# Kernel optimization log

Hardware: AMD Instinct MI355X
Metric: run time of the kernel (lower is better)

Reference implementation:

```python
import jax, jax.numpy as jnp
import numpy as np

M, A, E, H = 2048, 64, 128, 256
NUM_BOND_TYPES, NUM_ATOM_TYPES = 4, 118

def setup_inputs() -> dict:
    key = jax.random.key(0)
    ks = jax.random.split(key, 12)
    s = 0.02
    return {
        'node_rep': jax.random.normal(ks[0], (M, A, H), jnp.float32),
        'edge_index': jax.random.randint(ks[1], (M, 2, E), 0, A, jnp.int32),
        'bond_type_target': jax.random.randint(ks[2], (M, E), 0, NUM_BOND_TYPES, jnp.int32),
        'atom_type_target': jax.random.randint(ks[3], (M, A), 0, NUM_ATOM_TYPES, jnp.int32),
        'Wp1': jax.random.normal(ks[4], (H, H), jnp.float32) * s, 'bp1': jnp.zeros((H,), jnp.float32),
        'Wp2': jax.random.normal(ks[5], (H, H), jnp.float32) * s, 'bp2': jnp.zeros((H,), jnp.float32),
        'Wb1': jax.random.normal(ks[6], (2 * H, H), jnp.float32) * s, 'bb1': jnp.zeros((H,), jnp.float32),
        'Wb2': jax.random.normal(ks[7], (H, NUM_BOND_TYPES), jnp.float32) * s, 'bb2': jnp.zeros((NUM_BOND_TYPES,), jnp.float32),
        'Wa1': jax.random.normal(ks[8], (H, H), jnp.float32) * s, 'ba1': jnp.zeros((H,), jnp.float32),
        'Wa2': jax.random.normal(ks[9], (H, NUM_ATOM_TYPES), jnp.float32) * s, 'ba2': jnp.zeros((NUM_ATOM_TYPES,), jnp.float32),
    }

def _mlp(x, W1, b1, W2, b2):
    return jnp.maximum(x @ W1 + b1, 0.0) @ W2 + b2

def reference(node_rep, edge_index, bond_type_target, atom_type_target,
              Wp1, bp1, Wp2, bp2, Wb1, bb1, Wb2, bb2, Wa1, ba1, Wa2, ba2):
    # bond_if_proj: per-atom 2-layer MLP (dropout=0 -> identity)  [M,A,H]
    proj = _mlp(node_rep, Wp1, bp1, Wp2, bp2)
    # gather bond endpoint reps: index_select over atoms per molecule  [M,E,H]
    start = jnp.take_along_axis(proj, edge_index[:, 0, :, None], axis=1)
    end = jnp.take_along_axis(proj, edge_index[:, 1, :, None], axis=1)
    bt_in = jnp.concatenate([start, end], axis=-1)            # [M,E,2H]
    bt_logits = _mlp(bt_in, Wb1, bb1, Wb2, bb2)               # [M,E,4]
    bt_logp = jax.nn.log_softmax(bt_logits, axis=-1)
    # per-molecule mean CE averaged over molecules == global mean (equal sizes)
    bond_type_loss = -jnp.mean(jnp.take_along_axis(bt_logp, bond_type_target[..., None], axis=-1))
    bond_type_acc = jnp.mean((jnp.argmax(bt_logits, axis=-1) == bond_type_target).astype(jnp.float32))
    # atom type classifier on raw node reps  [M,A,118]
    at_logits = _mlp(node_rep, Wa1, ba1, Wa2, ba2)
    at_logp = jax.nn.log_softmax(at_logits, axis=-1)
    atom_type_loss = -jnp.mean(jnp.take_along_axis(at_logp, atom_type_target[..., None], axis=-1))
    atom_type_acc = jnp.mean((jnp.argmax(at_logits, axis=-1) == atom_type_target).astype(jnp.float32))
    loss = 0.5 * bond_type_loss + 0.5 * atom_type_loss
    return loss, bond_type_acc, atom_type_acc
```

## Files before the change

kernel.cpp:

```cpp
#include <hip/hip_runtime.h>
#include <hip/hip_bf16.h>

typedef __bf16 bf16x8 __attribute__((ext_vector_type(8)));
typedef float f32x16 __attribute__((ext_vector_type(16)));

__device__ inline unsigned short f2bf(float f) {
  __hip_bfloat16 h = __float2bfloat16(f);
  return *reinterpret_cast<unsigned short*>(&h);
}
__device__ inline unsigned pack2bf(float a, float b) {
  return (unsigned)f2bf(a) | ((unsigned)f2bf(b) << 16);
}
__device__ inline uint2 pack4bf(float a, float b, float c, float d) {
  uint2 r; r.x = pack2bf(a, b); r.y = pack2bf(c, d); return r;
}
__device__ inline bf16x8 as_bf16x8(uint4 v) { return __builtin_bit_cast(bf16x8, v); }
__device__ inline float bitf(unsigned u) { return __builtin_bit_cast(float, u); }
__device__ inline f32x16 mfma16(bf16x8 a, bf16x8 b, f32x16 c) {
  return __builtin_amdgcn_mfma_f32_32x32x16_bf16(a, b, c, 0, 0, 0);
}

#define BADDR(XB, R, KK)                                                       \
  ((XB) + (((((R) * 32 + l31) << 9) + ((KK) << 5) + (h << 4)) ^ swz))

#define GEMMM(XB, W1PTR, W2PTR, CW_)                                           \
  {                                                                            \
    const unsigned char* w1_ = (const unsigned char*)(W1PTR) +                 \
                               (((CW_) + l31) << 5) + (h << 4);                \
    const unsigned char* w2_ = (const unsigned char*)(W2PTR) +                 \
                               (((CW_) + l31) << 5) + (h << 4);                \
    u00 = zero; u01 = zero; u10 = zero; u11 = zero;                            \
    v00 = zero; v01 = zero; v10 = zero; v11 = zero;                            \
    bf16x8 pB0 = *(const bf16x8*)BADDR(XB, 0, 0);                              \
    bf16x8 pB1 = *(const bf16x8*)BADDR(XB, 1, 0);                              \
    uint4 pA0 = *(const uint4*)(w1_ + 0);                                      \
    uint4 pA1 = *(const uint4*)(w1_ + 1024);                                   \
    uint4 pC0 = *(const uint4*)(w2_ + 0);                                      \
    uint4 pC1 = *(const uint4*)(w2_ + 1024);                                   \
    _Pragma("clang loop unroll(disable)")                                      \
    for (int kk = 0; kk < 16; kk += 2) {                                       \
      bf16x8 qB0 = *(const bf16x8*)BADDR(XB, 0, kk + 1);                       \
      bf16x8 qB1 = *(const bf16x8*)BADDR(XB, 1, kk + 1);                       \
      uint4 qA0 = *(const uint4*)(w1_ + ((kk + 1) << 13));                     \
      uint4 qA1 = *(const uint4*)(w1_ + ((kk + 1) << 13) + 1024);              \
      uint4 qC0 = *(const uint4*)(w2_ + ((kk + 1) << 13));                     \
      uint4 qC1 = *(const uint4*)(w2_ + ((kk + 1) << 13) + 1024);              \
      u00 = mfma16(as_bf16x8(pA0), pB0, u00);                                  \
      u10 = mfma16(as_bf16x8(pA1), pB0, u10);                                  \
      u01 = mfma16(as_bf16x8(pA0), pB1, u01);                                  \
      u11 = mfma16(as_bf16x8(pA1), pB1, u11);                                  \
      v00 = mfma16(as_bf16x8(pC0), pB0, v00);                                  \
      v10 = mfma16(as_bf16x8(pC1), pB0, v10);                                  \
      v01 = mfma16(as_bf16x8(pC0), pB1, v01);                                  \
      v11 = mfma16(as_bf16x8(pC1), pB1, v11);                                  \
      if (kk + 2 < 16) {                                                       \
        pB0 = *(const bf16x8*)BADDR(XB, 0, kk + 2);                            \
        pB1 = *(const bf16x8*)BADDR(XB, 1, kk + 2);                            \
        pA0 = *(const uint4*)(w1_ + ((kk + 2) << 13));                         \
        pA1 = *(const uint4*)(w1_ + ((kk + 2) << 13) + 1024);                  \
        pC0 = *(const uint4*)(w2_ + ((kk + 2) << 13));                         \
        pC1 = *(const uint4*)(w2_ + ((kk + 2) << 13) + 1024);                  \
      }                                                                        \
      u00 = mfma16(as_bf16x8(qA0), qB0, u00);                                  \
      u10 = mfma16(as_bf16x8(qA1), qB0, u10);                                  \
      u01 = mfma16(as_bf16x8(qA0), qB1, u01);                                  \
      u11 = mfma16(as_bf16x8(qA1), qB1, u11);                                  \
      v00 = mfma16(as_bf16x8(qC0), qB0, v00);                                  \
      v10 = mfma16(as_bf16x8(qC1), qB0, v10);                                  \
      v01 = mfma16(as_bf16x8(qC0), qB1, v01);                                  \
      v11 = mfma16(as_bf16x8(qC1), qB1, v11);                                  \
    }                                                                          \
  }

#define WB22(DB, ACC, R, C, CW_, BIASPTR)                                      \
  _Pragma("unroll")                                                            \
  for (int g = 0; g < 4; ++g) {                                                \
    int xr_ = (R) * 32 + l31;                                                  \
    int col = (CW_) + (C) * 32 + g * 8 + h * 4;                                \
    float4 bb = *(const float4*)((BIASPTR) + col);                             \
    float v0 = fmaxf(ACC[4 * g + 0] + bb.x, 0.f);                              \
    float v1 = fmaxf(ACC[4 * g + 1] + bb.y, 0.f);                              \
    float v2 = fmaxf(ACC[4 * g + 2] + bb.z, 0.f);                              \
    float v3 = fmaxf(ACC[4 * g + 3] + bb.w, 0.f);                              \
    int off = ((xr_ << 9) + (col << 1)) ^ ((xr_ & 7) << 4);                    \
    *(uint2*)((DB) + off) = pack4bf(v0, v1, v2, v3);                           \
  }

#define WB22R(DB, ACC, R, C, CW_)                                              \
  _Pragma("unroll")                                                            \
  for (int g = 0; g < 4; ++g) {                                                \
    int xr_ = (R) * 32 + l31;                                                  \
    int col = (CW_) + (C) * 32 + g * 8 + h * 4;                                \
    int off = ((xr_ << 9) + (col << 1)) ^ ((xr_ & 7) << 4);                    \
    *(uint2*)((DB) + off) = pack4bf(ACC[4 * g + 0], ACC[4 * g + 1],            \
                                    ACC[4 * g + 2], ACC[4 * g + 3]);           \
  }

#define STAGE_X(DST, SRC)                                                      \
  _Pragma("unroll")                                                            \
  for (int it = 0; it < 8; ++it) {                                             \
    int lb = (it * 256 + tid) * 16;                                            \
    int d_ = lb ^ (((lb >> 9) & 7) << 4);                                      \
    const float4* s4 = (const float4*)((SRC) + (lb >> 1));                     \
    float4 f0 = s4[0], f1 = s4[1];                                             \
    uint4 v_ = { pack2bf(f0.x, f0.y), pack2bf(f0.z, f0.w),                     \
                 pack2bf(f1.x, f1.y), pack2bf(f1.z, f1.w) };                   \
    *(uint4*)((DST) + d_) = v_;                                                \
  }

__global__ __launch_bounds__(256) void k_pack(
    const float* __restrict__ wp1, const float* __restrict__ wa1,
    const float* __restrict__ wa2,
    unsigned short* __restrict__ dp1, unsigned short* __restrict__ da1,
    unsigned short* __restrict__ da2, float* __restrict__ accum)
{
  int b = blockIdx.x, tid = threadIdx.x;
  if (b == 0 && tid < 8) accum[tid] = 0.f;
  const float* src; unsigned short* dst; int e, logN, Nreal;
  if (b < 256)       { src = wp1; dst = dp1; e = b * 256 + tid;          logN = 8; Nreal = 256; }
  else if (b < 512)  { src = wa1; dst = da1; e = (b - 256) * 256 + tid;  logN = 8; Nreal = 256; }
  else               { src = wa2; dst = da2; e = (b - 512) * 256 + tid;  logN = 7; Nreal = 118; }
  int dk = e & 15;
  int rest = e >> 4;
  int n = rest & ((1 << logN) - 1);
  int kk = rest >> logN;
  int k = kk * 16 + dk;
  float v = (n < Nreal) ? src[k * Nreal + n] : 0.f;
  dst[e] = f2bf(v);
}

__global__ __launch_bounds__(256) void k_fold(
    const float* __restrict__ wp2, const float* __restrict__ wb1,
    const float* __restrict__ bp2, const float* __restrict__ bb1,
    unsigned short* __restrict__ dct, unsigned short* __restrict__ dcb,
    float* __restrict__ bias_e)
{
  int b = blockIdx.x, n = threadIdx.x;
  if (b < 512) {
    int k = b & 255;
    int off = (b < 256) ? 0 : 256;
    float s = 0.f;
    for (int t = 0; t < 256; ++t)
      s += wp2[k * 256 + t] * wb1[(t + off) * 256 + n];
    unsigned short* dst = (b < 256) ? dct : dcb;
    dst[((k >> 4) * 256 + n) * 16 + (k & 15)] = f2bf(s);
  } else {
    float s = bb1[n];
    for (int t = 0; t < 256; ++t)
      s += bp2[t] * (wb1[t * 256 + n] + wb1[(256 + t) * 256 + n]);
    bias_e[n] = s;
  }
}

__global__ __launch_bounds__(256, 2) void k_mol(
    const float* __restrict__ node, const int* __restrict__ eidx,
    const int* __restrict__ btt, const int* __restrict__ att,
    const unsigned short* __restrict__ wp1p, const float* __restrict__ bp1,
    const unsigned short* __restrict__ wctp, const unsigned short* __restrict__ wcbp,
    const float* __restrict__ bias_e, const float* __restrict__ wb2,
    const float* __restrict__ bb2,
    const unsigned short* __restrict__ wa1p, const float* __restrict__ ba1,
    const unsigned short* __restrict__ wa2p, const float* __restrict__ ba2,
    float* __restrict__ accum)
{
  __shared__ __align__(16) unsigned char bufA[32768];
  __shared__ __align__(16) unsigned char bufB[32768];
  __shared__ float s_bias[256];
  __shared__ float4 s_wb2[256];
  __shared__ float s_b2a[128];
  __shared__ float s_red[8];
  const int tid = threadIdx.x;
  const int lane = tid & 63;
  const int w = tid >> 6;
  const int l31 = lane & 31;
  const int h = lane >> 5;
  const int swz = (l31 & 7) << 4;
  const int CW = w * 64;
  const int m = blockIdx.x;

  STAGE_X(bufA, node + (long)m * 16384);
  s_bias[tid] = bias_e[tid];
  s_wb2[tid] = ((const float4*)wb2)[tid];
  if (tid < 128) s_b2a[tid] = (tid < 118) ? ba2[tid] : 0.f;
  const int t_at = att[m * 64 + (tid >> 2)];
  __syncthreads();

  f32x16 zero = {};
  f32x16 u00, u01, u10, u11, v00, v01, v10, v11;

  GEMMM(bufA, wa1p, wp1p, CW);
  WB22(bufB, u00, 0, 0, CW, ba1);
  WB22(bufB, u10, 0, 1, CW, ba1);
  WB22(bufB, u01, 1, 0, CW, ba1);
  WB22(bufB, u11, 1, 1, CW, ba1);
  __syncthreads();
  WB22(bufA, v00, 0, 0, CW, bp1);
  WB22(bufA, v10, 0, 1, CW, bp1);
  WB22(bufA, v01, 1, 0, CW, bp1);
  WB22(bufA, v11, 1, 1, CW, bp1);
  __syncthreads();

  f32x16 accL0 = zero, accL1 = zero;
  {
    const int cw2 = w * 32;
    const unsigned char* wb_ = (const unsigned char*)wa2p +
                               ((cw2 + l31) << 5) + (h << 4);
    bf16x8 pB0 = *(const bf16x8*)BADDR(bufB, 0, 0);
    bf16x8 pB1 = *(const bf16x8*)BADDR(bufB, 1, 0);
    uint4 pA = *(const uint4*)(wb_);
    _Pragma("clang loop unroll(disable)")
    for (int kk = 0; kk < 16; kk += 2) {
      bf16x8 qB0 = *(const bf16x8*)BADDR(bufB, 0, kk + 1);
      bf16x8 qB1 = *(const bf16x8*)BADDR(bufB, 1, kk + 1);
      uint4 qA = *(const uint4*)(wb_ + ((kk + 1) << 12));
      accL0 = mfma16(as_bf16x8(pA), pB0, accL0);
      accL1 = mfma16(as_bf16x8(pA), pB1, accL1);
      if (kk + 2 < 16) {
        pB0 = *(const bf16x8*)BADDR(bufB, 0, kk + 2);
        pB1 = *(const bf16x8*)BADDR(bufB, 1, kk + 2);
        pA = *(const uint4*)(wb_ + ((kk + 2) << 12));
      }
      accL0 = mfma16(as_bf16x8(qA), qB0, accL0);
      accL1 = mfma16(as_bf16x8(qA), qB1, accL1);
    }
  }
  __syncthreads();

  {
    const int cw2 = w * 32;
    #pragma unroll
    for (int q = 0; q < 16; ++q) {
      int col = cw2 + (q & 3) + 8 * (q >> 2) + 4 * h;
      if (col < 118) {
        float bv = s_b2a[col];
        int r0 = l31, r1 = 32 + l31;
        *(float*)(bufB + ((r0 << 9) + (((col << 2)) ^ ((r0 & 7) << 4)))) = accL0[q] + bv;
        *(float*)(bufB + ((r1 << 9) + (((col << 2)) ^ ((r1 & 7) << 4)))) = accL1[q] + bv;
      }
    }
  }
  __syncthreads();

  {
    const int row = tid >> 2, g4 = tid & 3;
    const int t = t_at;
    const unsigned char* lr = bufB + (row << 9);
    const int rswz = (row & 7) << 4;
    const int c0 = g4 * 30;
    const int cend = (g4 == 3) ? 118 : c0 + 30;
    float mx = -3.0e38f; int am = 127;
    for (int c = c0; c < cend; ++c) {
      float v = *(const float*)(lr + (((c << 2)) ^ rswz));
      if (v > mx) { mx = v; am = c; }
    }
    float mo = __shfl_xor(mx, 1); int amo = __shfl_xor(am, 1);
    if (mo > mx || (mo == mx && amo < am)) { mx = mo; am = amo; }
    mo = __shfl_xor(mx, 2); amo = __shfl_xor(am, 2);
    if (mo > mx || (mo == mx && amo < am)) { mx = mo; am = amo; }
    float s = 0.f, vt = 0.f;
    for (int c = c0; c < cend; ++c) {
      float v = *(const float*)(lr + (((c << 2)) ^ rswz));
      s += __expf(v - mx);
      if (c == t) vt = v;
    }
    s += __shfl_xor(s, 1); s += __shfl_xor(s, 2);
    vt += __shfl_xor(vt, 1); vt += __shfl_xor(vt, 2);
    float ce = 0.f, cc = 0.f;
    if (g4 == 0) { ce = __logf(s) + mx - vt; cc = (am == t) ? 1.f : 0.f; }
    #pragma unroll
    for (int d = 1; d < 64; d <<= 1) { ce += __shfl_xor(ce, d); cc += __shfl_xor(cc, d); }
    if (lane == 0) { s_red[w * 2] = ce; s_red[w * 2 + 1] = cc; }
  }

  GEMMM(bufA, wctp, wcbp, CW);
  const int es = eidx[m * 256 + (tid >> 1)];
  const int ed = eidx[m * 256 + 128 + (tid >> 1)];
  const int etg = btt[m * 128 + (tid >> 1)];
  const float b20 = bb2[0], b21 = bb2[1], b22 = bb2[2], b23 = bb2[3];
  __syncthreads();
  if (tid == 0) {
    atomicAdd(accum + 2, s_red[0] + s_red[2] + s_red[4] + s_red[6]);
    atomicAdd(accum + 3, s_red[1] + s_red[3] + s_red[5] + s_red[7]);
  }
  WB22R(bufA, u00, 0, 0, CW);
  WB22R(bufA, u10, 0, 1, CW);
  WB22R(bufA, u01, 1, 0, CW);
  WB22R(bufA, u11, 1, 1, CW);
  WB22R(bufB, v00, 0, 0, CW);
  WB22R(bufB, v10, 0, 1, CW);
  WB22R(bufB, v01, 1, 0, CW);
  WB22R(bufB, v11, 1, 1, CW);
  __syncthreads();

  {
    const int hf = tid & 1;
    float lg0 = 0.f, lg1 = 0.f, lg2 = 0.f, lg3 = 0.f;
    #pragma unroll
    for (int j = 0; j < 16; ++j) {
      int c0 = hf * 128 + j * 8;
      int offS = ((es << 9) + (c0 << 1)) ^ ((es & 7) << 4);
      int offD = ((ed << 9) + (c0 << 1)) ^ ((ed & 7) << 4);
      uint4 us = *(const uint4*)(bufA + offS);
      uint4 ud = *(const uint4*)(bufB + offD);
      const unsigned* pu = (const unsigned*)&us;
      const unsigned* pv = (const unsigned*)&ud;
      #pragma unroll
      for (int q = 0; q < 4; ++q) {
        unsigned ua = pu[q], ub = pv[q];
        int c = c0 + 2 * q;
        float hlo = bitf(ua << 16) + bitf(ub << 16) + s_bias[c];
        float hhi = bitf(ua & 0xffff0000u) + bitf(ub & 0xffff0000u) + s_bias[c + 1];
        hlo = fmaxf(hlo, 0.f); hhi = fmaxf(hhi, 0.f);
        float4 w0 = s_wb2[c], w1 = s_wb2[c + 1];
        lg0 = fmaf(hlo, w0.x, fmaf(hhi, w1.x, lg0));
        lg1 = fmaf(hlo, w0.y, fmaf(hhi, w1.y, lg1));
        lg2 = fmaf(hlo, w0.z, fmaf(hhi, w1.z, lg2));
        lg3 = fmaf(hlo, w0.w, fmaf(hhi, w1.w, lg3));
      }
    }
    lg0 += __shfl_xor(lg0, 1); lg1 += __shfl_xor(lg1, 1);
    lg2 += __shfl_xor(lg2, 1); lg3 += __shfl_xor(lg3, 1);
    float ce = 0.f, cc = 0.f;
    if (hf == 0) {
      float l0 = lg0 + b20, l1 = lg1 + b21, l2 = lg2 + b22, l3 = lg3 + b23;
      int t = etg;
      int am = 0; float mx = l0;
      if (l1 > mx) { mx = l1; am = 1; }
      if (l2 > mx) { mx = l2; am = 2; }
      if (l3 > mx) { mx = l3; am = 3; }
      float s = __expf(l0 - mx) + __expf(l1 - mx) + __expf(l2 - mx) + __expf(l3 - mx);
      float lt = (t == 0) ? l0 : (t == 1) ? l1 : (t == 2) ? l2 : l3;
      ce = __logf(s) + mx - lt;
      cc = (am == t) ? 1.f : 0.f;
    }
    #pragma unroll
    for (int d = 1; d < 64; d <<= 1) { ce += __shfl_xor(ce, d); cc += __shfl_xor(cc, d); }
    if (lane == 0) { s_red[w * 2] = ce; s_red[w * 2 + 1] = cc; }
    __syncthreads();
    if (tid == 0) {
      atomicAdd(accum + 0, s_red[0] + s_red[2] + s_red[4] + s_red[6]);
      atomicAdd(accum + 1, s_red[1] + s_red[3] + s_red[5] + s_red[7]);
    }
  }
}

__global__ __launch_bounds__(64) void k_final(const float* __restrict__ accum,
                                              float* __restrict__ out)
{
  if (threadIdx.x == 0) {
    float bce = accum[0] / 262144.f;
    float bcc = accum[1] / 262144.f;
    float ace = accum[2] / 131072.f;
    float acc_ = accum[3] / 131072.f;
    out[0] = 0.5f * bce + 0.5f * ace;
    out[1] = bcc;
    out[2] = acc_;
  }
}

extern "C" void kernel_launch(void* const* d_in, const int* in_sizes, int n_in,
                              void* d_out, int out_size, void* d_ws, size_t ws_size,
                              hipStream_t stream)
{
  const float* node = (const float*)d_in[0];
  const int* eidx   = (const int*)d_in[1];
  const int* btt    = (const int*)d_in[2];
  const int* att    = (const int*)d_in[3];
  const float* Wp1 = (const float*)d_in[4];
  const float* bp1 = (const float*)d_in[5];
  const float* Wp2 = (const float*)d_in[6];
  const float* bp2 = (const float*)d_in[7];
  const float* Wb1 = (const float*)d_in[8];
  const float* bb1 = (const float*)d_in[9];
  const float* Wb2 = (const float*)d_in[10];
  const float* bb2 = (const float*)d_in[11];
  const float* Wa1 = (const float*)d_in[12];
  const float* ba1 = (const float*)d_in[13];
  const float* Wa2 = (const float*)d_in[14];
  const float* ba2 = (const float*)d_in[15];

  char* ws = (char*)d_ws;
  float* accum = (float*)ws;
  unsigned short* dp1 = (unsigned short*)(ws + 256);
  unsigned short* da1 = (unsigned short*)(ws + 131328);
  unsigned short* da2 = (unsigned short*)(ws + 262400);
  unsigned short* dct = (unsigned short*)(ws + 327936);
  unsigned short* dcb = (unsigned short*)(ws + 459008);
  float* bias_e       = (float*)(ws + 590080);

  k_pack<<<640, 256, 0, stream>>>(Wp1, Wa1, Wa2, dp1, da1, da2, accum);
  k_fold<<<513, 256, 0, stream>>>(Wp2, Wb1, bp2, bb1, dct, dcb, bias_e);
  k_mol<<<2048, 256, 0, stream>>>(node, eidx, btt, att, dp1, bp1, dct, dcb,
                                  bias_e, Wb2, bb2, da1, ba1, da2, ba2, accum);
  k_final<<<1, 64, 0, stream>>>(accum, (float*)d_out);
}
```

Baseline: 205.7 us.

## Split per-molecule work across 8 waves with 2x4 row/column warp tiling

```diff
diff --git a/kernel.cpp b/kernel.cpp
--- a/kernel.cpp
+++ b/kernel.cpp
@@ -20,77 +20,65 @@
   return __builtin_amdgcn_mfma_f32_32x32x16_bf16(a, b, c, 0, 0, 0);
 }
 
-#define BADDR(XB, R, KK)                                                       \
-  ((XB) + (((((R) * 32 + l31) << 9) + ((KK) << 5) + (h << 4)) ^ swz))
-
-#define GEMMM(XB, W1PTR, W2PTR, CW_)                                           \
+#define BROW(XB, KK)                                                           \
+  ((XB) + ((((rw + l31) << 9) + ((KK) << 5) + (h << 4)) ^ swz))
+
+#define GEMM8(XB, W1PTR, W2PTR)                                                \
   {                                                                            \
     const unsigned char* w1_ = (const unsigned char*)(W1PTR) +                 \
-                               (((CW_) + l31) << 5) + (h << 4);                \
+                               ((cw + l31) << 5) + (h << 4);                   \
     const unsigned char* w2_ = (const unsigned char*)(W2PTR) +                 \
-                               (((CW_) + l31) << 5) + (h << 4);                \
-    u00 = zero; u01 = zero; u10 = zero; u11 = zero;                            \
-    v00 = zero; v01 = zero; v10 = zero; v11 = zero;                            \
-    bf16x8 pB0 = *(const bf16x8*)BADDR(XB, 0, 0);                              \
-    bf16x8 pB1 = *(const bf16x8*)BADDR(XB, 1, 0);                              \
-    uint4 pA0 = *(const uint4*)(w1_ + 0);                                      \
+                               ((cw + l31) << 5) + (h << 4);                   \
+    u0 = zero; u1 = zero; v0 = zero; v1 = zero;                                \
+    bf16x8 pB = *(const bf16x8*)BROW(XB, 0);                                   \
+    uint4 pA0 = *(const uint4*)(w1_);                                          \
     uint4 pA1 = *(const uint4*)(w1_ + 1024);                                   \
-    uint4 pC0 = *(const uint4*)(w2_ + 0);                                      \
+    uint4 pC0 = *(const uint4*)(w2_);                                          \
     uint4 pC1 = *(const uint4*)(w2_ + 1024);                                   \
     _Pragma("clang loop unroll(disable)")                                      \
     for (int kk = 0; kk < 16; kk += 2) {                                       \
-      bf16x8 qB0 = *(const bf16x8*)BADDR(XB, 0, kk + 1);                       \
-      bf16x8 qB1 = *(const bf16x8*)BADDR(XB, 1, kk + 1);                       \
+      bf16x8 qB = *(const bf16x8*)BROW(XB, kk + 1);                            \
       uint4 qA0 = *(const uint4*)(w1_ + ((kk + 1) << 13));                     \
       uint4 qA1 = *(const uint4*)(w1_ + ((kk + 1) << 13) + 1024);              \
       uint4 qC0 = *(const uint4*)(w2_ + ((kk + 1) << 13));                     \
       uint4 qC1 = *(const uint4*)(w2_ + ((kk + 1) << 13) + 1024);              \
-      u00 = mfma16(as_bf16x8(pA0), pB0, u00);                                  \
-      u10 = mfma16(as_bf16x8(pA1), pB0, u10);                                  \
-      u01 = mfma16(as_bf16x8(pA0), pB1, u01);                                  \
-      u11 = mfma16(as_bf16x8(pA1), pB1, u11);                                  \
-      v00 = mfma16(as_bf16x8(pC0), pB0, v00);                                  \
-      v10 = mfma16(as_bf16x8(pC1), pB0, v10);                                  \
-      v01 = mfma16(as_bf16x8(pC0), pB1, v01);                                  \
-      v11 = mfma16(as_bf16x8(pC1), pB1, v11);                                  \
+      u0 = mfma16(as_bf16x8(pA0), pB, u0);                                     \
+      u1 = mfma16(as_bf16x8(pA1), pB, u1);                                     \
+      v0 = mfma16(as_bf16x8(pC0), pB, v0);                                     \
+      v1 = mfma16(as_bf16x8(pC1), pB, v1);                                     \
       if (kk + 2 < 16) {                                                       \
-        pB0 = *(const bf16x8*)BADDR(XB, 0, kk + 2);                            \
-        pB1 = *(const bf16x8*)BADDR(XB, 1, kk + 2);                            \
+        pB = *(const bf16x8*)BROW(XB, kk + 2);                                 \
         pA0 = *(const uint4*)(w1_ + ((kk + 2) << 13));                         \
         pA1 = *(const uint4*)(w1_ + ((kk + 2) << 13) + 1024);                  \
         pC0 = *(const uint4*)(w2_ + ((kk + 2) << 13));                         \
         pC1 = *(const uint4*)(w2_ + ((kk + 2) << 13) + 1024);                  \
       }                                                                        \
-      u00 = mfma16(as_bf16x8(qA0), qB0, u00);                                  \
-      u10 = mfma16(as_bf16x8(qA1), qB0, u10);                                  \
-      u01 = mfma16(as_bf16x8(qA0), qB1, u01);                                  \
-      u11 = mfma16(as_bf16x8(qA1), qB1, u11);                                  \
-      v00 = mfma16(as_bf16x8(qC0), qB0, v00);                                  \
-      v10 = mfma16(as_bf16x8(qC1), qB0, v10);                                  \
-      v01 = mfma16(as_bf16x8(qC0), qB1, v01);                                  \
-      v11 = mfma16(as_bf16x8(qC1), qB1, v11);                                  \
+      u0 = mfma16(as_bf16x8(qA0), qB, u0);                                     \
+      u1 = mfma16(as_bf16x8(qA1), qB, u1);                                     \
+      v0 = mfma16(as_bf16x8(qC0), qB, v0);                                     \
+      v1 = mfma16(as_bf16x8(qC1), qB, v1);                                     \
     }                                                                          \
   }
 
-#define WB22(DB, ACC, R, C, CW_, BIASPTR)                                      \
+#define WB8(DB, ACC, C, BIASPTR)                                               \
   _Pragma("unroll")                                                            \
   for (int g = 0; g < 4; ++g) {                                                \
-    int xr_ = (R) * 32 + l31;                                                  \
-    int col = (CW_) + (C) * 32 + g * 8 + h * 4;                                \
+    int xr_ = rw + l31;                                                        \
+    int col = cw + (C) * 32 + g * 8 + h * 4;                                   \
     float4 bb = *(const float4*)((BIASPTR) + col);                             \
-    float v0 = fmaxf(ACC[4 * g + 0] + bb.x, 0.f);                              \
-    float v1 = fmaxf(ACC[4 * g + 1] + bb.y, 0.f);                              \
-    float v2 = fmaxf(ACC[4 * g + 2] + bb.z, 0.f);                              \
-    float v3 = fmaxf(ACC[4 * g + 3] + bb.w, 0.f);                              \
+    float v0_ = fmaxf(ACC[4 * g + 0] + bb.x, 0.f);                             \
+    float v1_ = fmaxf(ACC[4 * g + 1] + bb.y, 0.f);                             \
+    float v2_ = fmaxf(ACC[4 * g + 2] + bb.z, 0.f);                             \
+    float v3_ = fmaxf(ACC[4 * g + 3] + bb.w, 0.f);                             \
     int off = ((xr_ << 9) + (col << 1)) ^ ((xr_ & 7) << 4);                    \
-    *(uint2*)((DB) + off) = pack4bf(v0, v1, v2, v3);                           \
-  }
-
-#define WB22R(DB, ACC, R, C, CW_)                                              \
+    *(uint2*)((DB) + off) = pack4bf(v0_, v1_, v2_, v3_);                       \
+  }
+
+#define WB8R(DB, ACC, C)                                                       \
   _Pragma("unroll")                                                            \
   for (int g = 0; g < 4; ++g) {                                                \
-    int xr_ = (R) * 32 + l31;                                                  \
-    int col = (CW_) + (C) * 32 + g * 8 + h * 4;                                \
+    int xr_ = rw + l31;                                                        \
+    int col = cw + (C) * 32 + g * 8 + h * 4;                                   \
     int off = ((xr_ << 9) + (col << 1)) ^ ((xr_ & 7) << 4);                    \
     *(uint2*)((DB) + off) = pack4bf(ACC[4 * g + 0], ACC[4 * g + 1],            \
                                     ACC[4 * g + 2], ACC[4 * g + 3]);           \
@@ -98,8 +86,8 @@
 
 #define STAGE_X(DST, SRC)                                                      \
   _Pragma("unroll")                                                            \
-  for (int it = 0; it < 8; ++it) {                                             \
-    int lb = (it * 256 + tid) * 16;                                            \
+  for (int it = 0; it < 4; ++it) {                                             \
+    int lb = (it * 512 + tid) * 16;                                            \
     int d_ = lb ^ (((lb >> 9) & 7) << 4);                                      \
     const float4* s4 = (const float4*)((SRC) + (lb >> 1));                     \
     float4 f0 = s4[0], f1 = s4[1];                                             \
@@ -152,7 +140,7 @@
   }
 }
 
-__global__ __launch_bounds__(256, 2) void k_mol(
+__global__ __launch_bounds__(512, 4) void k_mol(
     const float* __restrict__ node, const int* __restrict__ eidx,
     const int* __restrict__ btt, const int* __restrict__ att,
     const unsigned short* __restrict__ wp1p, const float* __restrict__ bp1,
@@ -168,136 +156,128 @@
   __shared__ float s_bias[256];
   __shared__ float4 s_wb2[256];
   __shared__ float s_b2a[128];
-  __shared__ float s_red[8];
+  __shared__ float s_red[16];
   const int tid = threadIdx.x;
   const int lane = tid & 63;
   const int w = tid >> 6;
   const int l31 = lane & 31;
   const int h = lane >> 5;
   const int swz = (l31 & 7) << 4;
-  const int CW = w * 64;
+  const int rw = (w >> 2) * 32;
+  const int cw = (w & 3) * 64;
   const int m = blockIdx.x;
 
   STAGE_X(bufA, node + (long)m * 16384);
-  s_bias[tid] = bias_e[tid];
-  s_wb2[tid] = ((const float4*)wb2)[tid];
+  if (tid < 256) {
+    s_bias[tid] = bias_e[tid];
+    s_wb2[tid] = ((const float4*)wb2)[tid];
+  }
   if (tid < 128) s_b2a[tid] = (tid < 118) ? ba2[tid] : 0.f;
-  const int t_at = att[m * 64 + (tid >> 2)];
+  const int t_at = att[m * 64 + (tid >> 3)];
   __syncthreads();
 
   f32x16 zero = {};
-  f32x16 u00, u01, u10, u11, v00, v01, v10, v11;
-
-  GEMMM(bufA, wa1p, wp1p, CW);
-  WB22(bufB, u00, 0, 0, CW, ba1);
-  WB22(bufB, u10, 0, 1, CW, ba1);
-  WB22(bufB, u01, 1, 0, CW, ba1);
-  WB22(bufB, u11, 1, 1, CW, ba1);
-  __syncthreads();
-  WB22(bufA, v00, 0, 0, CW, bp1);
-  WB22(bufA, v10, 0, 1, CW, bp1);
-  WB22(bufA, v01, 1, 0, CW, bp1);
-  WB22(bufA, v11, 1, 1, CW, bp1);
-  __syncthreads();
-
-  f32x16 accL0 = zero, accL1 = zero;
+  f32x16 u0, u1, v0, v1;
+
+  GEMM8(bufA, wa1p, wp1p);
+  WB8(bufB, u0, 0, ba1);
+  WB8(bufB, u1, 1, ba1);
+  __syncthreads();
+  WB8(bufA, v0, 0, bp1);
+  WB8(bufA, v1, 1, bp1);
+  __syncthreads();
+
+  f32x16 aL = zero;
   {
-    const int cw2 = w * 32;
+    const int cw2 = (w & 3) * 32;
     const unsigned char* wb_ = (const unsigned char*)wa2p +
                                ((cw2 + l31) << 5) + (h << 4);
-    bf16x8 pB0 = *(const bf16x8*)BADDR(bufB, 0, 0);
-    bf16x8 pB1 = *(const bf16x8*)BADDR(bufB, 1, 0);
+    bf16x8 pB = *(const bf16x8*)BROW(bufB, 0);
     uint4 pA = *(const uint4*)(wb_);
     _Pragma("clang loop unroll(disable)")
     for (int kk = 0; kk < 16; kk += 2) {
-      bf16x8 qB0 = *(const bf16x8*)BADDR(bufB, 0, kk + 1);
-      bf16x8 qB1 = *(const bf16x8*)BADDR(bufB, 1, kk + 1);
+      bf16x8 qB = *(const bf16x8*)BROW(bufB, kk + 1);
       uint4 qA = *(const uint4*)(wb_ + ((kk + 1) << 12));
-      accL0 = mfma16(as_bf16x8(pA), pB0, accL0);
-      accL1 = mfma16(as_bf16x8(pA), pB1, accL1);
+      aL = mfma16(as_bf16x8(pA), pB, aL);
       if (kk + 2 < 16) {
-        pB0 = *(const bf16x8*)BADDR(bufB, 0, kk + 2);
-        pB1 = *(const bf16x8*)BADDR(bufB, 1, kk + 2);
+        pB = *(const bf16x8*)BROW(bufB, kk + 2);
         pA = *(const uint4*)(wb_ + ((kk + 2) << 12));
       }
-      accL0 = mfma16(as_bf16x8(qA), qB0, accL0);
-      accL1 = mfma16(as_bf16x8(qA), qB1, accL1);
+      aL = mfma16(as_bf16x8(qA), qB, aL);
     }
   }
   __syncthreads();
 
   {
-    const int cw2 = w * 32;
+    const int cw2 = (w & 3) * 32;
+    const int r0 = rw + l31;
     #pragma unroll
     for (int q = 0; q < 16; ++q) {
       int col = cw2 + (q & 3) + 8 * (q >> 2) + 4 * h;
-      if (col < 118) {
-        float bv = s_b2a[col];
-        int r0 = l31, r1 = 32 + l31;
-        *(float*)(bufB + ((r0 << 9) + (((col << 2)) ^ ((r0 & 7) << 4)))) = accL0[q] + bv;
-        *(float*)(bufB + ((r1 << 9) + (((col << 2)) ^ ((r1 & 7) << 4)))) = accL1[q] + bv;
-      }
+      if (col < 118)
+        *(float*)(bufB + ((r0 << 9) + (((col << 2)) ^ ((r0 & 7) << 4)))) =
+            aL[q] + s_b2a[col];
     }
   }
   __syncthreads();
 
   {
-    const int row = tid >> 2, g4 = tid & 3;
-    const int t = t_at;
+    const int row = tid >> 3, g8 = tid & 7;
     const unsigned char* lr = bufB + (row << 9);
     const int rswz = (row & 7) << 4;
-    const int c0 = g4 * 30;
-    const int cend = (g4 == 3) ? 118 : c0 + 30;
+    const int c0 = g8 * 15;
+    const int cend = (g8 == 7) ? 118 : c0 + 15;
     float mx = -3.0e38f; int am = 127;
     for (int c = c0; c < cend; ++c) {
       float v = *(const float*)(lr + (((c << 2)) ^ rswz));
       if (v > mx) { mx = v; am = c; }
     }
-    float mo = __shfl_xor(mx, 1); int amo = __shfl_xor(am, 1);
-    if (mo > mx || (mo == mx && amo < am)) { mx = mo; am = amo; }
-    mo = __shfl_xor(mx, 2); amo = __shfl_xor(am, 2);
-    if (mo > mx || (mo == mx && amo < am)) { mx = mo; am = amo; }
+    #pragma unroll
+    for (int d = 1; d < 8; d <<= 1) {
+      float mo = __shfl_xor(mx, d); int amo = __shfl_xor(am, d);
+      if (mo > mx || (mo == mx && amo < am)) { mx = mo; am = amo; }
+    }
     float s = 0.f, vt = 0.f;
     for (int c = c0; c < cend; ++c) {
       float v = *(const float*)(lr + (((c << 2)) ^ rswz));
       s += __expf(v - mx);
-      if (c == t) vt = v;
-    }
-    s += __shfl_xor(s, 1); s += __shfl_xor(s, 2);
-    vt += __shfl_xor(vt, 1); vt += __shfl_xor(vt, 2);
+      if (c == t_at) vt = v;
+    }
+    #pragma unroll
+    for (int d = 1; d < 8; d <<= 1) { s += __shfl_xor(s, d); vt += __shfl_xor(vt, d); }
     float ce = 0.f, cc = 0.f;
-    if (g4 == 0) { ce = __logf(s) + mx - vt; cc = (am == t) ? 1.f : 0.f; }
-    #pragma unroll
-    for (int d = 1; d < 64; d <<= 1) { ce += __shfl_xor(ce, d); cc += __shfl_xor(cc, d); }
+    if (g8 == 0) { ce = __logf(s) + mx - vt; cc = (am == t_at) ? 1.f : 0.f; }
+    #pragma unroll
+    for (int d = 8; d < 64; d <<= 1) { ce += __shfl_xor(ce, d); cc += __shfl_xor(cc, d); }
+    #pragma unroll
+    for (int d = 1; d < 8; d <<= 1) { ce += __shfl_xor(ce, d); cc += __shfl_xor(cc, d); }
     if (lane == 0) { s_red[w * 2] = ce; s_red[w * 2 + 1] = cc; }
   }
 
-  GEMMM(bufA, wctp, wcbp, CW);
-  const int es = eidx[m * 256 + (tid >> 1)];
-  const int ed = eidx[m * 256 + 128 + (tid >> 1)];
-  const int etg = btt[m * 128 + (tid >> 1)];
+  GEMM8(bufA, wctp, wcbp);
+  const int es = eidx[m * 256 + (tid >> 2)];
+  const int ed = eidx[m * 256 + 128 + (tid >> 2)];
+  const int etg = btt[m * 128 + (tid >> 2)];
   const float b20 = bb2[0], b21 = bb2[1], b22 = bb2[2], b23 = bb2[3];
   __syncthreads();
   if (tid == 0) {
-    atomicAdd(accum + 2, s_red[0] + s_red[2] + s_red[4] + s_red[6]);
-    atomicAdd(accum + 3, s_red[1] + s_red[3] + s_red[5] + s_red[7]);
-  }
-  WB22R(bufA, u00, 0, 0, CW);
-  WB22R(bufA, u10, 0, 1, CW);
-  WB22R(bufA, u01, 1, 0, CW);
-  WB22R(bufA, u11, 1, 1, CW);
-  WB22R(bufB, v00, 0, 0, CW);
-  WB22R(bufB, v10, 0, 1, CW);
-  WB22R(bufB, v01, 1, 0, CW);
-  WB22R(bufB, v11, 1, 1, CW);
+    atomicAdd(accum + 2, s_red[0] + s_red[2] + s_red[4] + s_red[6] +
+                         s_red[8] + s_red[10] + s_red[12] + s_red[14]);
+    atomicAdd(accum + 3, s_red[1] + s_red[3] + s_red[5] + s_red[7] +
+                         s_red[9] + s_red[11] + s_red[13] + s_red[15]);
+  }
+  WB8R(bufA, u0, 0);
+  WB8R(bufA, u1, 1);
+  WB8R(bufB, v0, 0);
+  WB8R(bufB, v1, 1);
   __syncthreads();
 
   {
-    const int hf = tid & 1;
+    const int qf = tid & 3;
     float lg0 = 0.f, lg1 = 0.f, lg2 = 0.f, lg3 = 0.f;
     #pragma unroll
-    for (int j = 0; j < 16; ++j) {
-      int c0 = hf * 128 + j * 8;
+    for (int j = 0; j < 8; ++j) {
+      int c0 = qf * 64 + j * 8;
       int offS = ((es << 9) + (c0 << 1)) ^ ((es & 7) << 4);
       int offD = ((ed << 9) + (c0 << 1)) ^ ((ed & 7) << 4);
       uint4 us = *(const uint4*)(bufA + offS);
@@ -320,8 +300,10 @@
     }
     lg0 += __shfl_xor(lg0, 1); lg1 += __shfl_xor(lg1, 1);
     lg2 += __shfl_xor(lg2, 1); lg3 += __shfl_xor(lg3, 1);
+    lg0 += __shfl_xor(lg0, 2); lg1 += __shfl_xor(lg1, 2);
+    lg2 += __shfl_xor(lg2, 2); lg3 += __shfl_xor(lg3, 2);
     float ce = 0.f, cc = 0.f;
-    if (hf == 0) {
+    if (qf == 0) {
       float l0 = lg0 + b20, l1 = lg1 + b21, l2 = lg2 + b22, l3 = lg3 + b23;
       int t = etg;
       int am = 0; float mx = l0;
@@ -338,8 +320,10 @@
     if (lane == 0) { s_red[w * 2] = ce; s_red[w * 2 + 1] = cc; }
     __syncthreads();
     if (tid == 0) {
-      atomicAdd(accum + 0, s_red[0] + s_red[2] + s_red[4] + s_red[6]);
-      atomicAdd(accum + 1, s_red[1] + s_red[3] + s_red[5] + s_red[7]);
+      atomicAdd(accum + 0, s_red[0] + s_red[2] + s_red[4] + s_red[6] +
+                           s_red[8] + s_red[10] + s_red[12] + s_red[14]);
+      atomicAdd(accum + 1, s_red[1] + s_red[3] + s_red[5] + s_red[7] +
+                           s_red[9] + s_red[11] + s_red[13] + s_red[15]);
     }
   }
 }
@@ -390,7 +374,7 @@
 
   k_pack<<<640, 256, 0, stream>>>(Wp1, Wa1, Wa2, dp1, da1, da2, accum);
   k_fold<<<513, 256, 0, stream>>>(Wp2, Wb1, bp2, bb1, dct, dcb, bias_e);
-  k_mol<<<2048, 256, 0, stream>>>(node, eidx, btt, att, dp1, bp1, dct, dcb,
+  k_mol<<<2048, 512, 0, stream>>>(node, eidx, btt, att, dp1, bp1, dct, dcb,
                                   bias_e, Wb2, bb2, da1, ba1, da2, ba2, accum);
   k_final<<<1, 64, 0, stream>>>(accum, (float*)d_out);
 }
```

After: 188.6 us (median of 2 runs). 8.3% less time.
